# Optimization experiments

Hardware: AMD Instinct MI355X
Metric: run time of the kernel (lower is better)

Reference implementation:

```python
import jax, jax.numpy as jnp
import numpy as np

_EPS = 1e-5

def _ln(x, g, b):
    m = jnp.mean(x, axis=-1, keepdims=True)
    v = jnp.var(x, axis=-1, keepdims=True)
    return (x - m) * jax.lax.rsqrt(v + _EPS) * g + b

def setup_inputs() -> dict:
    key = jax.random.key(0)
    ks = jax.random.split(key, 12)
    B, S, D = 8, 2048, 1024
    H = 2 * D          # hidden_dim = 2*n_embd
    A = H // 16        # adapt_dim = 128
    E = 8              # num_experts
    std = 1.0 / D ** 0.5
    astd = std * 0.01
    f = lambda k, shape, s: jax.random.normal(k, shape, dtype=jnp.float32) * s
    return {
        'x': f(ks[0], (B, S, D), 1.0),
        'expert_weights': f(ks[1], (B, S, E), 1.0),
        'w_up': f(ks[2], (H, D), std),
        'w_gate': f(ks[3], (H, D), std),
        'w_down': f(ks[4], (D, H), std),
        'w_pre': f(ks[5], (A, D), astd),
        'w_post': f(ks[6], (A, H), astd),
        'an_g': jnp.ones((A,), jnp.float32),
        'an_b': jnp.zeros((A,), jnp.float32),
        'w_aproj': f(ks[7], (H, A), astd),
        'w_exp': f(ks[8], (E, A, A), 0.01 / A ** 0.5),
        'eln_g': jnp.ones((E, A), jnp.float32),
        'eln_b': jnp.zeros((E, A), jnp.float32),
        'w_eproj': f(ks[9], (H, A), 0.01 / A ** 0.5),
        'w_out': f(ks[10], (D, H), 0.01 / A ** 0.5),
    }

def reference(x, expert_weights, w_up, w_gate, w_down, w_pre, w_post,
              an_g, an_b, w_aproj, w_exp, eln_g, eln_b, w_eproj, w_out):
    # ---- shared LLaDAExpert ----
    up = jnp.einsum('bsd,hd->bsh', x, w_up)
    gate = jnp.einsum('bsd,hd->bsh', x, w_gate)
    hidden = jax.nn.silu(gate) * up                      # [B,S,H]
    pre = jnp.einsum('bsd,ad->bsa', x, w_pre)            # pre_adapt(x), reused by experts
    adapt_in = _ln(pre, an_g, an_b)                      # [B,S,A]
    adapt_out = _ln(jnp.einsum('bsh,ah->bsa', hidden, w_post), an_g, an_b)
    aw = jax.nn.silu(jnp.clip(jnp.einsum('bsa,bta->bst', adapt_in, adapt_out), -5.0, 5.0))  # [B,S,S]
    adapt = jnp.einsum('bst,bta->bsa', aw, adapt_in)     # [B,S,A]
    hidden = hidden + 0.1 * jnp.einsum('bsa,ha->bsh', adapt, w_aproj)
    shared = jnp.einsum('bsh,dh->bsd', hidden, w_down)   # [B,S,D]
    combined = jnp.zeros_like(shared)
    E = w_exp.shape[0]
    for i in range(E):
        a = _ln(jnp.einsum('bsa,ca->bsc', pre, w_exp[i]), eln_g[i], eln_b[i])
        o = jnp.einsum('bsh,dh->bsd', jnp.einsum('bsc,hc->bsh', a, w_eproj), w_out)
        mask = expert_weights[:, :, i] > 0
        combined = jnp.where(mask[..., None], o, combined)
    return shared + 0.1 * combined
```

## Files before the change

kernel.cpp:

```cpp
#include <hip/hip_runtime.h>

#define TOK 16384
#define DD 1024
#define HH 2048
#define AA 128
#define EE 8
#define SS 2048
#define BB 8

typedef __attribute__((ext_vector_type(8))) short short8;
typedef __attribute__((ext_vector_type(4))) float floatx4;

__device__ __forceinline__ unsigned short f2b(float f) {
  unsigned u = __float_as_uint(f);
  u += 0x7fff + ((u >> 16) & 1);
  return (unsigned short)(u >> 16);
}
__device__ __forceinline__ float b2f(unsigned short h) {
  return __uint_as_float(((unsigned)h) << 16);
}

__device__ __forceinline__ void xcd_swizzle(int& bx, int& by) {
  const int nbx = gridDim.x, nby = gridDim.y;
  if ((nby & 7) == 0) {
    const int L = blockIdx.y * nbx + blockIdx.x;
    const int xcd = L & 7, idx = L >> 3;
    bx = idx % nbx;
    by = (xcd * (nby >> 3)) + idx / nbx;
  } else {
    bx = blockIdx.x; by = blockIdx.y;
  }
}


__device__ __forceinline__ void gload16(const short* g, short* l) {
  __builtin_amdgcn_global_load_lds((__attribute__((address_space(1))) void*)(void*)g,
                                   (__attribute__((address_space(3))) void*)l, 16, 0, 0);
}

__device__ __forceinline__ void stage_tile(const short* src, int ld, short* dst, int wave) {
#pragma unroll
  for (int i = 0; i < 4; ++i)
    gload16(src + (long)i*64*ld, dst + i*4096 + wave*512);
}

__device__ __forceinline__ void ktile256(const char* Ab, const char* Bb,
                                         short* Ad, short* Bd,
                                         const short* nA, int nlda,
                                         const short* nB, int nldb,
                                         bool st, int wave,
                                         int aOff, int bOff, int slot0, int slot1,
                                         floatx4 (*acc)[4])
{
  short8 af[4][2], bf[4][2];
#pragma unroll
  for (int m = 0; m < 4; ++m) {
    af[m][0] = *(const short8*)(Ab + aOff + m*2048 + slot0);
    af[m][1] = *(const short8*)(Ab + aOff + m*2048 + slot1);
  }
#pragma unroll
  for (int n = 0; n < 2; ++n) {
    bf[n][0] = *(const short8*)(Bb + bOff + n*2048 + slot0);
    bf[n][1] = *(const short8*)(Bb + bOff + n*2048 + slot1);
  }
  __builtin_amdgcn_s_barrier();
  asm volatile("s_waitcnt lgkmcnt(0)" ::: "memory");
  __builtin_amdgcn_s_setprio(1);
#pragma unroll
  for (int m = 0; m < 4; ++m)
#pragma unroll
    for (int n = 0; n < 2; ++n) {
      acc[m][n] = __builtin_amdgcn_mfma_f32_16x16x32_bf16(af[m][0], bf[n][0], acc[m][n], 0, 0, 0);
      acc[m][n] = __builtin_amdgcn_mfma_f32_16x16x32_bf16(af[m][1], bf[n][1], acc[m][n], 0, 0, 0);
    }
  __builtin_amdgcn_s_setprio(0);
  __builtin_amdgcn_s_barrier();
#pragma unroll
  for (int n = 2; n < 4; ++n) {
    bf[n][0] = *(const short8*)(Bb + bOff + n*2048 + slot0);
    bf[n][1] = *(const short8*)(Bb + bOff + n*2048 + slot1);
  }
  __builtin_amdgcn_s_barrier();
  asm volatile("s_waitcnt lgkmcnt(0)" ::: "memory");
  __builtin_amdgcn_s_setprio(1);
#pragma unroll
  for (int m = 0; m < 4; ++m)
#pragma unroll
    for (int n = 2; n < 4; ++n) {
      acc[m][n] = __builtin_amdgcn_mfma_f32_16x16x32_bf16(af[m][0], bf[n][0], acc[m][n], 0, 0, 0);
      acc[m][n] = __builtin_amdgcn_mfma_f32_16x16x32_bf16(af[m][1], bf[n][1], acc[m][n], 0, 0, 0);
    }
  __builtin_amdgcn_s_setprio(0);
  __builtin_amdgcn_s_barrier();
#pragma unroll
  for (int m = 0; m < 4; ++m) {
    af[m][0] = *(const short8*)(Ab + aOff + (m+4)*2048 + slot0);
    af[m][1] = *(const short8*)(Ab + aOff + (m+4)*2048 + slot1);
  }
  if (st) stage_tile(nB, nldb, Bd, wave);
  __builtin_amdgcn_s_barrier();
  asm volatile("s_waitcnt lgkmcnt(0)" ::: "memory");
  __builtin_amdgcn_s_setprio(1);
#pragma unroll
  for (int m = 0; m < 4; ++m)
#pragma unroll
    for (int n = 0; n < 2; ++n) {
      acc[m+4][n] = __builtin_amdgcn_mfma_f32_16x16x32_bf16(af[m][0], bf[n][0], acc[m+4][n], 0, 0, 0);
      acc[m+4][n] = __builtin_amdgcn_mfma_f32_16x16x32_bf16(af[m][1], bf[n][1], acc[m+4][n], 0, 0, 0);
    }
  __builtin_amdgcn_s_setprio(0);
  __builtin_amdgcn_s_barrier();
  if (st) stage_tile(nA, nlda, Ad, wave);
  __builtin_amdgcn_s_barrier();
  __builtin_amdgcn_s_setprio(1);
#pragma unroll
  for (int m = 0; m < 4; ++m)
#pragma unroll
    for (int n = 2; n < 4; ++n) {
      acc[m+4][n] = __builtin_amdgcn_mfma_f32_16x16x32_bf16(af[m][0], bf[n][0], acc[m+4][n], 0, 0, 0);
      acc[m+4][n] = __builtin_amdgcn_mfma_f32_16x16x32_bf16(af[m][1], bf[n][1], acc[m+4][n], 0, 0, 0);
    }
  __builtin_amdgcn_s_setprio(0);
  if (st) asm volatile("s_waitcnt vmcnt(8)" ::: "memory");
  else    asm volatile("s_waitcnt vmcnt(0)" ::: "memory");
  __builtin_amdgcn_s_barrier();
}

template<int EPI>
__global__ __launch_bounds__(512, 2)
void gemm256(const unsigned short* __restrict__ Ag, int lda,
             const unsigned short* __restrict__ Bg, int ldb,
             void* __restrict__ Cg, int ldc,
             const unsigned short* __restrict__ Xg, int ldx,
             int K1,
             const unsigned short* __restrict__ A2g, int lda2,
             const unsigned short* __restrict__ B2g, int ldb2,
             int K2)
{
  __shared__ __align__(16) short As[2][256*64];
  __shared__ __align__(16) short Bs[2][256*64];
  int bx, by; xcd_swizzle(bx, by);
  const int tid = threadIdx.x;
  const int lane = tid & 63, wave = tid >> 6;
  const int q = lane >> 4, l15 = lane & 15;
  const int wm = wave >> 2, wn = wave & 3;

  const int arow = tid >> 3;
  const int kc8  = ((tid & 7) ^ (arow & 7)) * 8;

  const short* a1 = (const short*)Ag + (long)(by*256 + arow)*lda + kc8;
  const short* b1 = (const short*)Bg + (long)(bx*256 + arow)*ldb + kc8;
  const short* a2 = A2g ? (const short*)A2g + (long)(by*256 + arow)*lda2 + kc8 : (const short*)0;
  const short* b2 = B2g ? (const short*)B2g + (long)(bx*256 + arow)*ldb2 + kc8 : (const short*)0;
  const int nt1 = K1 >> 6, nt = (K1 + K2) >> 6, niter = nt >> 1;

  auto tA = [&](int T, const short*& p, int& ld) {
    if (T < nt1) { p = a1 + T*64; ld = lda; } else { p = a2 + (T - nt1)*64; ld = lda2; }
  };
  auto tB = [&](int T, const short*& p, int& ld) {
    if (T < nt1) { p = b1 + T*64; ld = ldb; } else { p = b2 + (T - nt1)*64; ld = ldb2; }
  };

  const int aOff  = (wm*128 + l15) * 128;
  const int bOff  = (wn*64  + l15) * 128;
  const int l7    = l15 & 7;
  const int slot0 = ((0*4 + q) ^ l7) * 16;
  const int slot1 = ((1*4 + q) ^ l7) * 16;

  floatx4 acc[8][4] = {};

  stage_tile(a1, lda, As[0], wave);
  stage_tile(b1, ldb, Bs[0], wave);
  {
    const short *pa, *pb; int la, lb;
    tA(1, pa, la); tB(1, pb, lb);
    stage_tile(pa, la, As[1], wave);
    stage_tile(pb, lb, Bs[1], wave);
  }
  asm volatile("s_waitcnt vmcnt(8)" ::: "memory");
  __builtin_amdgcn_s_barrier();

  for (int i = 0; i < niter; ++i) {
    const int t2 = 2*i + 2;
    const bool st = t2 < nt;
    const short *na = a1, *nb = b1; int nla = lda, nlb = ldb;
    if (st) { tA(t2, na, nla); tB(t2, nb, nlb); }
    ktile256((const char*)As[0], (const char*)Bs[0], As[0], Bs[0],
             na, nla, nb, nlb, st, wave, aOff, bOff, slot0, slot1, acc);
    if (st) { tA(t2+1, na, nla); tB(t2+1, nb, nlb); }
    ktile256((const char*)As[1], (const char*)Bs[1], As[1], Bs[1],
             na, nla, nb, nlb, st, wave, aOff, bOff, slot0, slot1, acc);
  }

#pragma unroll
  for (int m = 0; m < 8; ++m)
#pragma unroll
    for (int n = 0; n < 4; ++n)
#pragma unroll
      for (int r = 0; r < 4; ++r) {
        const int row = by*256 + wm*128 + m*16 + q*4 + r;
        const int col = bx*256 + wn*64  + n*16 + l15;
        const long ci = (long)row*ldc + col;
        float v = acc[m][n][r];
        if (EPI == 0) {
          ((float*)Cg)[ci] = v;
        } else if (EPI == 1) {
          v = v / (1.f + __expf(-v));
          ((unsigned short*)Cg)[ci] = f2b(v);
        } else if (EPI == 2) {
          float g = b2f(Xg[(long)row*ldx + col]);
          ((unsigned short*)Cg)[ci] = f2b(v * g);
        }
      }
}

__device__ __forceinline__ void kloop_pipe(const short* Ap, int lda, const short* Bp, int ldb,
                                           short* As, short* Bs, int K,
                                           int tid, int q, int l15, int l7, int wm, int wn,
                                           floatx4 (*acc)[4])
{
  short8 pa[4], pb[4];
#pragma unroll
  for (int i = 0; i < 4; ++i) {
    pa[i] = *(const short8*)(Ap + (long)i*32*lda);
    pb[i] = *(const short8*)(Bp + (long)i*32*ldb);
  }
  for (int kt = 0; kt < K; kt += 64) {
#pragma unroll
    for (int i = 0; i < 4; ++i) {
      *(short8*)((char*)As + i*4096 + tid*16) = pa[i];
      *(short8*)((char*)Bs + i*4096 + tid*16) = pb[i];
    }
    __syncthreads();
    if (kt + 64 < K) {
#pragma unroll
      for (int i = 0; i < 4; ++i) {
        pa[i] = *(const short8*)(Ap + (long)i*32*lda + kt + 64);
        pb[i] = *(const short8*)(Bp + (long)i*32*ldb + kt + 64);
      }
    }
#pragma unroll
    for (int s = 0; s < 2; ++s) {
      short8 af[4], bf[4];
      const int slotoff = ((s*4 + q) ^ l7) * 16;
#pragma unroll
      for (int i = 0; i < 4; ++i) {
        af[i] = *(const short8*)((const char*)As + (wm*64 + i*16 + l15)*128 + slotoff);
        bf[i] = *(const short8*)((const char*)Bs + (wn*64 + i*16 + l15)*128 + slotoff);
      }
#pragma unroll
      for (int i = 0; i < 4; ++i)
#pragma unroll
        for (int j = 0; j < 4; ++j)
          acc[i][j] = __builtin_amdgcn_mfma_f32_16x16x32_bf16(af[i], bf[j], acc[i][j], 0, 0, 0);
    }
    __syncthreads();
  }
}

__global__ void cast_f32_bf16(const float* __restrict__ in, unsigned short* __restrict__ out, long n4) {
  long i = (long)blockIdx.x * blockDim.x + threadIdx.x;
  const long stride = (long)gridDim.x * blockDim.x;
  for (; i < n4; i += stride) {
    float4 v = ((const float4*)in)[i];
    ushort4 o;
    o.x = f2b(v.x); o.y = f2b(v.y); o.z = f2b(v.z); o.w = f2b(v.w);
    ((ushort4*)out)[i] = o;
  }
}

__global__ void transpose_cast(const float* __restrict__ in, unsigned short* __restrict__ out,
                               int R, int C) {
  __shared__ float t[32][33];
  const int lx = threadIdx.x & 31, ly = threadIdx.x >> 5;
  const int r0 = blockIdx.y * 32, c0 = blockIdx.x * 32;
#pragma unroll
  for (int i = 0; i < 32; i += 8)
    t[ly + i][lx] = in[(long)(r0 + ly + i) * C + (c0 + lx)];
  __syncthreads();
#pragma unroll
  for (int i = 0; i < 32; i += 8)
    out[(long)(c0 + ly + i) * R + (r0 + lx)] = f2b(t[lx][ly + i]);
}

template<int EPI>
__global__ __launch_bounds__(256)
void gemm_bt(const unsigned short* __restrict__ Ag, long sAz, int lda,
             const unsigned short* __restrict__ Bg, long sBz, int ldb,
             void* __restrict__ Cg, long sCz, int ldc,
             const unsigned short* __restrict__ Xg, long sXz, int ldx,
             int K)
{
  __shared__ __align__(16) short As[128*64];
  __shared__ __align__(16) short Bs[128*64];
  int bx, by; xcd_swizzle(bx, by);
  const int tid  = threadIdx.x;
  const int lane = tid & 63, wave = tid >> 6;
  const int q = lane >> 4, l15 = lane & 15, l7 = lane & 7;
  const int wm = wave & 1, wn = wave >> 1;

  const int arow = tid >> 3;
  const int kc8  = ((tid & 7) ^ (arow & 7)) * 8;

  const short* Ap = (const short*)Ag + (long)blockIdx.z*sAz + (long)(by*128 + arow)*lda + kc8;
  const short* Bp = (const short*)Bg + (long)blockIdx.z*sBz + (long)(bx*128 + arow)*ldb + kc8;

  floatx4 acc[4][4] = {};
  kloop_pipe(Ap, lda, Bp, ldb, As, Bs, K, tid, q, l15, l7, wm, wn, acc);

  const long cz = (long)blockIdx.z * sCz;
  const long xz = (long)blockIdx.z * sXz;
#pragma unroll
  for (int i = 0; i < 4; ++i)
#pragma unroll
    for (int j = 0; j < 4; ++j)
#pragma unroll
      for (int r = 0; r < 4; ++r) {
        const int row = by*128 + wm*64 + i*16 + q*4 + r;
        const int col = bx*128 + wn*64 + j*16 + l15;
        const long ci = cz + (long)row*ldc + col;
        float v = acc[i][j][r];
        if (EPI == 0) {
          ((float*)Cg)[ci] = v;
        } else if (EPI == 1) {
          v = v / (1.f + __expf(-v));
          ((unsigned short*)Cg)[ci] = f2b(v);
        } else if (EPI == 2) {
          float g = b2f(Xg[xz + (long)row*ldx + col]);
          ((unsigned short*)Cg)[ci] = f2b(v * g);
        } else if (EPI == 3) {
          ((unsigned short*)Cg)[ci] = f2b(v);
        } else if (EPI == 4) {
          v = fminf(fmaxf(v, -5.f), 5.f);
          v = v / (1.f + __expf(-v));
          ((unsigned short*)Cg)[ci] = f2b(v);
        } else if (EPI == 6) {
          ((unsigned short*)Cg)[ci] = f2b(0.1f * v);
        }
      }
}

__global__ void ln_rows(const float* __restrict__ X, const float* __restrict__ g,
                        const float* __restrict__ b, unsigned short* __restrict__ lnout,
                        unsigned short* __restrict__ rawout, unsigned short* __restrict__ tout)
{
  const int lane = threadIdx.x & 63, wave = threadIdx.x >> 6;
  const long t = (long)blockIdx.x*4 + wave;
  const float* x = X + t*AA;
  float x0 = x[lane], x1 = x[lane + 64];
  float s = x0 + x1, s2 = x0*x0 + x1*x1;
#pragma unroll
  for (int m = 1; m < 64; m <<= 1) {
    s  += __shfl_xor(s, m, 64);
    s2 += __shfl_xor(s2, m, 64);
  }
  float mean = s * (1.f/AA);
  float inv  = rsqrtf(s2*(1.f/AA) - mean*mean + 1e-5f);
  float y0 = (x0 - mean)*inv*g[lane] + b[lane];
  float y1 = (x1 - mean)*inv*g[lane+64] + b[lane+64];
  lnout[t*AA + lane]      = f2b(y0);
  lnout[t*AA + lane + 64] = f2b(y1);
  if (rawout) { rawout[t*AA+lane] = f2b(x0); rawout[t*AA+lane+64] = f2b(x1); }
  if (tout) {
    const long bb = t >> 11, si = t & (SS-1);
    tout[bb*(long)AA*SS + (long)lane*SS + si]      = f2b(y0);
    tout[bb*(long)AA*SS + (long)(lane+64)*SS + si] = f2b(y1);
  }
}

__global__ void expert_select_ln(const float* __restrict__ ew, const unsigned short* __restrict__ eall,
                                 const float* __restrict__ eg, const float* __restrict__ ebias,
                                 unsigned short* __restrict__ Fc)
{
  const int lane = threadIdx.x & 63, wave = threadIdx.x >> 6;
  const long t = (long)blockIdx.x*4 + wave;
  const float* w = ew + t*EE;
  int ie = -1;
#pragma unroll
  for (int i = 0; i < EE; ++i) if (w[i] > 0.f) ie = i;
  unsigned short o0 = 0, o1 = 0;
  if (ie >= 0) {
    float x0 = b2f(eall[t*(EE*AA) + ie*AA + lane]);
    float x1 = b2f(eall[t*(EE*AA) + ie*AA + lane + 64]);
    float s = x0 + x1, s2 = x0*x0 + x1*x1;
#pragma unroll
    for (int m = 1; m < 64; m <<= 1) { s += __shfl_xor(s, m, 64); s2 += __shfl_xor(s2, m, 64); }
    float mean = s * (1.f/AA);
    float inv  = rsqrtf(s2*(1.f/AA) - mean*mean + 1e-5f);
    o0 = f2b((x0-mean)*inv*eg[ie*AA+lane]    + ebias[ie*AA+lane]);
    o1 = f2b((x1-mean)*inv*eg[ie*AA+lane+64] + ebias[ie*AA+lane+64]);
  }
  Fc[t*256 + lane]      = o0;
  Fc[t*256 + lane + 64] = o1;
}

extern "C" void kernel_launch(void* const* d_in, const int* in_sizes, int n_in,
                              void* d_out, int out_size, void* d_ws, size_t ws_size,
                              hipStream_t stream)
{
  const float* x       = (const float*)d_in[0];
  const float* ew      = (const float*)d_in[1];
  const float* w_up    = (const float*)d_in[2];
  const float* w_gate  = (const float*)d_in[3];
  const float* w_down  = (const float*)d_in[4];
  const float* w_pre   = (const float*)d_in[5];
  const float* w_post  = (const float*)d_in[6];
  const float* an_g    = (const float*)d_in[7];
  const float* an_b    = (const float*)d_in[8];
  const float* w_aproj = (const float*)d_in[9];
  const float* w_exp   = (const float*)d_in[10];
  const float* eln_g   = (const float*)d_in[11];
  const float* eln_b   = (const float*)d_in[12];
  const float* w_eproj = (const float*)d_in[13];
  const float* w_out   = (const float*)d_in[14];

  char* ws = (char*)d_ws;
  size_t off = 0;
  auto take = [&](size_t bytes) { char* p = ws + off; off += (bytes + 255) & ~(size_t)255; return p; };

  unsigned short* Sc    = (unsigned short*)take((size_t)BB*SS*SS*2);
  unsigned short* xb    = Sc;
  unsigned short* eall  = (unsigned short*)((char*)Sc + (size_t)TOK*DD*2);
  unsigned short* hid   = (unsigned short*)take((size_t)TOK*HH*2);
  float*          pre   = (float*)take((size_t)TOK*AA*4);
  float*          postA = (float*)take((size_t)TOK*AA*4);
  unsigned short* Fc    = (unsigned short*)take((size_t)TOK*256*2);
  unsigned short* ain   = (unsigned short*)take((size_t)TOK*AA*2);
  unsigned short* ainT  = (unsigned short*)take((size_t)TOK*AA*2);
  unsigned short* aout  = (unsigned short*)take((size_t)TOK*AA*2);
  unsigned short* preb  = (unsigned short*)take((size_t)TOK*AA*2);
  unsigned short* wgb   = (unsigned short*)take((size_t)HH*DD*2);
  unsigned short* wub   = (unsigned short*)take((size_t)HH*DD*2);
  unsigned short* wdb   = (unsigned short*)take((size_t)DD*HH*2);
  unsigned short* wpostb= (unsigned short*)take((size_t)AA*HH*2);
  unsigned short* wpreb = (unsigned short*)take((size_t)AA*DD*2);
  unsigned short* wexpb = (unsigned short*)take((size_t)EE*AA*AA*2);
  unsigned short* Wc    = (unsigned short*)take((size_t)DD*256*2);
  (void)ws_size; (void)in_sizes; (void)n_in; (void)out_size;

  unsigned short* woutb  = hid;
  unsigned short* btT    = hid + (size_t)DD*HH;
  unsigned short* eprojT = btT;
  unsigned short* aprojT = btT + (size_t)AA*HH;

  cast_f32_bf16<<<1024, 256, 0, stream>>>(x,      xb,     (long)TOK*DD/4);
  cast_f32_bf16<<<256,  256, 0, stream>>>(w_gate, wgb,    (long)HH*DD/4);
  cast_f32_bf16<<<256,  256, 0, stream>>>(w_up,   wub,    (long)HH*DD/4);
  cast_f32_bf16<<<256,  256, 0, stream>>>(w_down, wdb,    (long)DD*HH/4);
  cast_f32_bf16<<<256,  256, 0, stream>>>(w_out,  woutb,  (long)DD*HH/4);
  cast_f32_bf16<<<64,   256, 0, stream>>>(w_post, wpostb, (long)AA*HH/4);
  cast_f32_bf16<<<32,   256, 0, stream>>>(w_pre,  wpreb,  (long)AA*DD/4);
  cast_f32_bf16<<<32,   256, 0, stream>>>(w_exp,  wexpb,  (long)EE*AA*AA/4);

  transpose_cast<<<dim3(AA/32, HH/32), 256, 0, stream>>>(w_eproj, eprojT, HH, AA);
  transpose_cast<<<dim3(AA/32, HH/32), 256, 0, stream>>>(w_aproj, aprojT, HH, AA);

  gemm_bt<6><<<dim3(1, DD/128, 2), 256, 0, stream>>>(
      woutb, (long)(wdb - woutb), HH,
      eprojT, (long)AA*HH, HH,
      Wc, AA, 256, nullptr, 0, 0, HH);

  gemm256<1><<<dim3(HH/256, TOK/256), 512, 0, stream>>>(
      xb, DD, wgb, DD, hid, HH, nullptr, 0, DD, nullptr, 0, nullptr, 0, 0);
  gemm256<2><<<dim3(HH/256, TOK/256), 512, 0, stream>>>(
      xb, DD, wub, DD, hid, HH, hid, HH, DD, nullptr, 0, nullptr, 0, 0);

  gemm_bt<0><<<dim3(1, TOK/128, 1), 256, 0, stream>>>(xb,0,DD, wpreb,0,DD, pre,0,AA, nullptr,0,0, DD);
  ln_rows<<<TOK/4, 256, 0, stream>>>(pre, an_g, an_b, ain, preb, ainT);

  gemm_bt<3><<<dim3((EE*AA)/128, TOK/128, 1), 256, 0, stream>>>(preb,0,AA, wexpb,0,AA, eall,0,EE*AA, nullptr,0,0, AA);
  expert_select_ln<<<TOK/4, 256, 0, stream>>>(ew, eall, eln_g, eln_b, Fc);

  gemm_bt<0><<<dim3(1, TOK/128, 1), 256, 0, stream>>>(hid,0,HH, wpostb,0,HH, postA,0,AA, nullptr,0,0, HH);
  ln_rows<<<TOK/4, 256, 0, stream>>>(postA, an_g, an_b, aout, nullptr, nullptr);

  gemm_bt<4><<<dim3(SS/128, SS/128, BB), 256, 0, stream>>>(ain,(long)SS*AA,AA, aout,(long)SS*AA,AA,
                                                           Sc,(long)SS*SS,SS, nullptr,0,0, AA);
  gemm_bt<3><<<dim3(1, SS/128, BB), 256, 0, stream>>>(Sc,(long)SS*SS,SS, ainT,(long)AA*SS,SS,
                                                      Fc+AA,(long)SS*256,256, nullptr,0,0, SS);
  gemm256<0><<<dim3(DD/256, TOK/256), 512, 0, stream>>>(
      hid, HH, wdb, HH, (float*)d_out, DD, nullptr, 0, HH, Fc, 256, Wc, 256, 256);
}
```

Measured before the change: 587.4 us.

## Software-pipeline LDS fragment reads across k-tiles in gemm256 main loop

Restructures the 256x256 GEMM inner k-tile so the LDS fragment loads for the next tile are issued during the last MFMA blocks of the current one, with fragments kept in registers across calls. The change removes several barriers and lgkmcnt waits per k-tile and overlaps LDS reads with MFMA work. It also adds a SEG2 template flag so the single-segment GEMMs drop the runtime check for a second K segment. In exchange it raises register pressure from holding 8x2 A and 4x2 B fragments, and it changes the vmcnt wait counts, which affects pipeline correctness.

```diff
diff --git a/kernel.cpp b/kernel.cpp
--- a/kernel.cpp
+++ b/kernel.cpp
@@ -44,89 +44,63 @@
     gload16(src + (long)i*64*ld, dst + i*4096 + wave*512);
 }
 
+#define MFMA_BLK(MM0, NN0)                                                               \
+  __builtin_amdgcn_s_setprio(1);                                                         \
+  _Pragma("unroll")                                                                      \
+  for (int m = 0; m < 4; ++m)                                                            \
+    _Pragma("unroll")                                                                    \
+    for (int n = 0; n < 2; ++n) {                                                        \
+      acc[MM0+m][NN0+n] = __builtin_amdgcn_mfma_f32_16x16x32_bf16(af[MM0+m][0], bf[NN0+n][0], acc[MM0+m][NN0+n], 0, 0, 0); \
+      acc[MM0+m][NN0+n] = __builtin_amdgcn_mfma_f32_16x16x32_bf16(af[MM0+m][1], bf[NN0+n][1], acc[MM0+m][NN0+n], 0, 0, 0); \
+    }                                                                                    \
+  __builtin_amdgcn_s_setprio(0);
+
 __device__ __forceinline__ void ktile256(const char* Ab, const char* Bb,
+                                         const char* An, const char* Bn,
                                          short* Ad, short* Bd,
-                                         const short* nA, int nlda,
-                                         const short* nB, int nldb,
-                                         bool st, int wave,
+                                         const short* sA, int slda,
+                                         const short* sB, int sldb,
+                                         bool st, bool rd, int wave,
                                          int aOff, int bOff, int slot0, int slot1,
+                                         short8 (&af)[8][2], short8 (&bf)[4][2],
                                          floatx4 (*acc)[4])
 {
-  short8 af[4][2], bf[4][2];
-#pragma unroll
-  for (int m = 0; m < 4; ++m) {
-    af[m][0] = *(const short8*)(Ab + aOff + m*2048 + slot0);
-    af[m][1] = *(const short8*)(Ab + aOff + m*2048 + slot1);
-  }
-#pragma unroll
-  for (int n = 0; n < 2; ++n) {
-    bf[n][0] = *(const short8*)(Bb + bOff + n*2048 + slot0);
-    bf[n][1] = *(const short8*)(Bb + bOff + n*2048 + slot1);
-  }
-  __builtin_amdgcn_s_barrier();
-  asm volatile("s_waitcnt lgkmcnt(0)" ::: "memory");
-  __builtin_amdgcn_s_setprio(1);
-#pragma unroll
-  for (int m = 0; m < 4; ++m)
-#pragma unroll
-    for (int n = 0; n < 2; ++n) {
-      acc[m][n] = __builtin_amdgcn_mfma_f32_16x16x32_bf16(af[m][0], bf[n][0], acc[m][n], 0, 0, 0);
-      acc[m][n] = __builtin_amdgcn_mfma_f32_16x16x32_bf16(af[m][1], bf[n][1], acc[m][n], 0, 0, 0);
-    }
-  __builtin_amdgcn_s_setprio(0);
-  __builtin_amdgcn_s_barrier();
 #pragma unroll
   for (int n = 2; n < 4; ++n) {
     bf[n][0] = *(const short8*)(Bb + bOff + n*2048 + slot0);
     bf[n][1] = *(const short8*)(Bb + bOff + n*2048 + slot1);
   }
+  MFMA_BLK(0, 0)
+#pragma unroll
+  for (int m = 4; m < 8; ++m) {
+    af[m][0] = *(const short8*)(Ab + aOff + m*2048 + slot0);
+    af[m][1] = *(const short8*)(Ab + aOff + m*2048 + slot1);
+  }
+  MFMA_BLK(0, 2)
+  asm volatile("s_waitcnt lgkmcnt(0)" ::: "memory");
   __builtin_amdgcn_s_barrier();
-  asm volatile("s_waitcnt lgkmcnt(0)" ::: "memory");
-  __builtin_amdgcn_s_setprio(1);
-#pragma unroll
-  for (int m = 0; m < 4; ++m)
-#pragma unroll
-    for (int n = 2; n < 4; ++n) {
-      acc[m][n] = __builtin_amdgcn_mfma_f32_16x16x32_bf16(af[m][0], bf[n][0], acc[m][n], 0, 0, 0);
-      acc[m][n] = __builtin_amdgcn_mfma_f32_16x16x32_bf16(af[m][1], bf[n][1], acc[m][n], 0, 0, 0);
-    }
-  __builtin_amdgcn_s_setprio(0);
-  __builtin_amdgcn_s_barrier();
-#pragma unroll
-  for (int m = 0; m < 4; ++m) {
-    af[m][0] = *(const short8*)(Ab + aOff + (m+4)*2048 + slot0);
-    af[m][1] = *(const short8*)(Ab + aOff + (m+4)*2048 + slot1);
-  }
-  if (st) stage_tile(nB, nldb, Bd, wave);
-  __builtin_amdgcn_s_barrier();
-  asm volatile("s_waitcnt lgkmcnt(0)" ::: "memory");
-  __builtin_amdgcn_s_setprio(1);
-#pragma unroll
-  for (int m = 0; m < 4; ++m)
-#pragma unroll
-    for (int n = 0; n < 2; ++n) {
-      acc[m+4][n] = __builtin_amdgcn_mfma_f32_16x16x32_bf16(af[m][0], bf[n][0], acc[m+4][n], 0, 0, 0);
-      acc[m+4][n] = __builtin_amdgcn_mfma_f32_16x16x32_bf16(af[m][1], bf[n][1], acc[m+4][n], 0, 0, 0);
-    }
-  __builtin_amdgcn_s_setprio(0);
-  __builtin_amdgcn_s_barrier();
-  if (st) stage_tile(nA, nlda, Ad, wave);
-  __builtin_amdgcn_s_barrier();
-  __builtin_amdgcn_s_setprio(1);
-#pragma unroll
-  for (int m = 0; m < 4; ++m)
-#pragma unroll
-    for (int n = 2; n < 4; ++n) {
-      acc[m+4][n] = __builtin_amdgcn_mfma_f32_16x16x32_bf16(af[m][0], bf[n][0], acc[m+4][n], 0, 0, 0);
-      acc[m+4][n] = __builtin_amdgcn_mfma_f32_16x16x32_bf16(af[m][1], bf[n][1], acc[m+4][n], 0, 0, 0);
-    }
-  __builtin_amdgcn_s_setprio(0);
-  if (st) asm volatile("s_waitcnt vmcnt(8)" ::: "memory");
+  if (st) stage_tile(sB, sldb, Bd, wave);
+  MFMA_BLK(4, 0)
+  if (st) asm volatile("s_waitcnt vmcnt(4)" ::: "memory");
   else    asm volatile("s_waitcnt vmcnt(0)" ::: "memory");
   __builtin_amdgcn_s_barrier();
-}
-
-template<int EPI>
+  if (rd) {
+#pragma unroll
+    for (int m = 0; m < 4; ++m) {
+      af[m][0] = *(const short8*)(An + aOff + m*2048 + slot0);
+      af[m][1] = *(const short8*)(An + aOff + m*2048 + slot1);
+    }
+#pragma unroll
+    for (int n = 0; n < 2; ++n) {
+      bf[n][0] = *(const short8*)(Bn + bOff + n*2048 + slot0);
+      bf[n][1] = *(const short8*)(Bn + bOff + n*2048 + slot1);
+    }
+  }
+  if (st) stage_tile(sA, slda, Ad, wave);
+  MFMA_BLK(4, 2)
+}
+
+template<int EPI, bool SEG2>
 __global__ __launch_bounds__(512, 2)
 void gemm256(const unsigned short* __restrict__ Ag, int lda,
              const unsigned short* __restrict__ Bg, int ldb,
@@ -150,15 +124,16 @@
 
   const short* a1 = (const short*)Ag + (long)(by*256 + arow)*lda + kc8;
   const short* b1 = (const short*)Bg + (long)(bx*256 + arow)*ldb + kc8;
-  const short* a2 = A2g ? (const short*)A2g + (long)(by*256 + arow)*lda2 + kc8 : (const short*)0;
-  const short* b2 = B2g ? (const short*)B2g + (long)(bx*256 + arow)*ldb2 + kc8 : (const short*)0;
-  const int nt1 = K1 >> 6, nt = (K1 + K2) >> 6, niter = nt >> 1;
+  const short* a2 = SEG2 ? (const short*)A2g + (long)(by*256 + arow)*lda2 + kc8 : (const short*)0;
+  const short* b2 = SEG2 ? (const short*)B2g + (long)(bx*256 + arow)*ldb2 + kc8 : (const short*)0;
+  const int nt1 = K1 >> 6, nt = SEG2 ? ((K1 + K2) >> 6) : (K1 >> 6);
+  const int niter = nt >> 1;
 
   auto tA = [&](int T, const short*& p, int& ld) {
-    if (T < nt1) { p = a1 + T*64; ld = lda; } else { p = a2 + (T - nt1)*64; ld = lda2; }
+    if (!SEG2 || T < nt1) { p = a1 + T*64; ld = lda; } else { p = a2 + (T - nt1)*64; ld = lda2; }
   };
   auto tB = [&](int T, const short*& p, int& ld) {
-    if (T < nt1) { p = b1 + T*64; ld = ldb; } else { p = b2 + (T - nt1)*64; ld = ldb2; }
+    if (!SEG2 || T < nt1) { p = b1 + T*64; ld = ldb; } else { p = b2 + (T - nt1)*64; ld = ldb2; }
   };
 
   const int aOff  = (wm*128 + l15) * 128;
@@ -180,16 +155,30 @@
   asm volatile("s_waitcnt vmcnt(8)" ::: "memory");
   __builtin_amdgcn_s_barrier();
 
+  short8 af[8][2], bf[4][2];
+#pragma unroll
+  for (int m = 0; m < 4; ++m) {
+    af[m][0] = *(const short8*)((const char*)As[0] + aOff + m*2048 + slot0);
+    af[m][1] = *(const short8*)((const char*)As[0] + aOff + m*2048 + slot1);
+  }
+#pragma unroll
+  for (int n = 0; n < 2; ++n) {
+    bf[n][0] = *(const short8*)((const char*)Bs[0] + bOff + n*2048 + slot0);
+    bf[n][1] = *(const short8*)((const char*)Bs[0] + bOff + n*2048 + slot1);
+  }
+
   for (int i = 0; i < niter; ++i) {
     const int t2 = 2*i + 2;
     const bool st = t2 < nt;
-    const short *na = a1, *nb = b1; int nla = lda, nlb = ldb;
-    if (st) { tA(t2, na, nla); tB(t2, nb, nlb); }
-    ktile256((const char*)As[0], (const char*)Bs[0], As[0], Bs[0],
-             na, nla, nb, nlb, st, wave, aOff, bOff, slot0, slot1, acc);
-    if (st) { tA(t2+1, na, nla); tB(t2+1, nb, nlb); }
-    ktile256((const char*)As[1], (const char*)Bs[1], As[1], Bs[1],
-             na, nla, nb, nlb, st, wave, aOff, bOff, slot0, slot1, acc);
+    const short *sa = a1, *sb = b1; int sla = lda, slb = ldb;
+    if (st) { tA(t2, sa, sla); tB(t2, sb, slb); }
+    ktile256((const char*)As[0], (const char*)Bs[0], (const char*)As[1], (const char*)Bs[1],
+             As[0], Bs[0], sa, sla, sb, slb, st, true, wave,
+             aOff, bOff, slot0, slot1, af, bf, acc);
+    if (st) { tA(t2+1, sa, sla); tB(t2+1, sb, slb); }
+    ktile256((const char*)As[1], (const char*)Bs[1], (const char*)As[0], (const char*)Bs[0],
+             As[1], Bs[1], sa, sla, sb, slb, st, st, wave,
+             aOff, bOff, slot0, slot1, af, bf, acc);
   }
 
 #pragma unroll
@@ -460,9 +449,9 @@
       eprojT, (long)AA*HH, HH,
       Wc, AA, 256, nullptr, 0, 0, HH);
 
-  gemm256<1><<<dim3(HH/256, TOK/256), 512, 0, stream>>>(
+  gemm256<1, false><<<dim3(HH/256, TOK/256), 512, 0, stream>>>(
       xb, DD, wgb, DD, hid, HH, nullptr, 0, DD, nullptr, 0, nullptr, 0, 0);
-  gemm256<2><<<dim3(HH/256, TOK/256), 512, 0, stream>>>(
+  gemm256<2, false><<<dim3(HH/256, TOK/256), 512, 0, stream>>>(
       xb, DD, wub, DD, hid, HH, hid, HH, DD, nullptr, 0, nullptr, 0, 0);
 
   gemm_bt<0><<<dim3(1, TOK/128, 1), 256, 0, stream>>>(xb,0,DD, wpreb,0,DD, pre,0,AA, nullptr,0,0, DD);
@@ -478,6 +467,6 @@
                                                            Sc,(long)SS*SS,SS, nullptr,0,0, AA);
   gemm_bt<3><<<dim3(1, SS/128, BB), 256, 0, stream>>>(Sc,(long)SS*SS,SS, ainT,(long)AA*SS,SS,
                                                       Fc+AA,(long)SS*256,256, nullptr,0,0, SS);
-  gemm256<0><<<dim3(DD/256, TOK/256), 512, 0, stream>>>(
+  gemm256<0, true><<<dim3(DD/256, TOK/256), 512, 0, stream>>>(
       hid, HH, wdb, HH, (float*)d_out, DD, nullptr, 0, HH, Fc, 256, Wc, 256, 256);
 }
```

Measured after the change: 610.7 us. 4.0% more time.
